# Kernel tuning notes

Measured on AMD Instinct MI355X. Metric: run time of the kernel, lower is better.

Reference implementation:

```python
import jax, jax.numpy as jnp
import numpy as np

TEMPERATURE = 0.1
EPS = 1e-12  # matches torch F.normalize default eps


def setup_inputs() -> dict:
    key = jax.random.key(0)
    k1, k2 = jax.random.split(key)
    B, D = 4096, 512
    features1 = jax.random.normal(k1, (B, D), dtype=jnp.float32)
    features2 = jax.random.normal(k2, (B, D), dtype=jnp.float32)
    return {"features1": features1, "features2": features2}


def _l2_normalize(x, axis=1):
    norm = jnp.linalg.norm(x, axis=axis, keepdims=True)
    return x / jnp.maximum(norm, EPS)


def reference(features1, features2):
    B = features1.shape[0]
    f1 = _l2_normalize(features1)
    f2 = _l2_normalize(features2)
    features = jnp.concatenate([f1, f2], axis=0)  # (2B, D)
    sim = jnp.matmul(features, features.T) / TEMPERATURE  # (2B, 2B)
    # mask self-similarity on the diagonal with -inf
    diag = jnp.eye(2 * B, dtype=bool)
    sim = jnp.where(diag, -jnp.inf, sim)
    # positive pair labels: row i pairs with i+B (first half) / i-B (second half)
    labels = jnp.concatenate([jnp.arange(B) + B, jnp.arange(B)], axis=0)
    log_probs = jax.nn.log_softmax(sim, axis=-1)  # (2B, 2B)
    nll = -jnp.take_along_axis(log_probs, labels[:, None], axis=1)[:, 0]
    return jnp.mean(nll)
```

## Files before the change

kernel.cpp:

```cpp
#include <hip/hip_runtime.h>

#define NROWS 8192
#define HALF_N 4096
#define DIM 512
#define INV_T 10.0f
#define NRB 64
#define NBLOCKS 2080

typedef __attribute__((ext_vector_type(4))) float f32x4;
typedef __attribute__((ext_vector_type(2))) long long2v;

__device__ __forceinline__ void async16(const void* g, void* l) {
  __builtin_amdgcn_global_load_lds(
      (const __attribute__((address_space(1))) unsigned int*)g,
      (__attribute__((address_space(3))) unsigned int*)l, 16, 0, 0);
}

__global__ __launch_bounds__(256) void norm_cast_k(
    const float* __restrict__ f1, const float* __restrict__ f2,
    unsigned char* __restrict__ Fn, float* __restrict__ rowsum) {
  int wave = threadIdx.x >> 6;
  int lane = threadIdx.x & 63;
  int row = blockIdx.x * 4 + wave;
  const float* src = (row < HALF_N) ? (f1 + (size_t)row * DIM)
                                    : (f2 + (size_t)(row - HALF_N) * DIM);
  const float4* p = reinterpret_cast<const float4*>(src + lane * 8);
  float4 v0 = p[0];
  float4 v1 = p[1];
  float ss = v0.x*v0.x + v0.y*v0.y + v0.z*v0.z + v0.w*v0.w
           + v1.x*v1.x + v1.y*v1.y + v1.z*v1.z + v1.w*v1.w;
  #pragma unroll
  for (int off = 1; off < 64; off <<= 1) ss += __shfl_xor(ss, off);
  float scale = 1.0f / fmaxf(sqrtf(ss), 1e-12f);
  int lo = __builtin_amdgcn_cvt_pk_fp8_f32(v0.x * scale, v0.y * scale, 0, false);
  lo = __builtin_amdgcn_cvt_pk_fp8_f32(v0.z * scale, v0.w * scale, lo, true);
  int u = lane & 7;
  int g = lane >> 3;
  int pos = 2 * (u & 3) + (u >> 2);
  *reinterpret_cast<int2*>(Fn + (size_t)row * DIM + g * 64 + pos * 8) =
      make_int2(lo,
                __builtin_amdgcn_cvt_pk_fp8_f32(v1.z * scale, v1.w * scale,
                    __builtin_amdgcn_cvt_pk_fp8_f32(v1.x * scale, v1.y * scale, 0, false),
                    true));
  if (lane == 0) rowsum[row] = 0.0f;
}

__global__ __launch_bounds__(256, 3) void sym_gemm_k(
    const unsigned char* __restrict__ Fn, float* __restrict__ rowsum,
    float* __restrict__ pairsim) {
  int bx = blockIdx.x;
  int gbx = (bx & 7) * (NBLOCKS / 8) + (bx >> 3);
  int rb = 0, rem = gbx;
  while (rem >= NRB - rb) { rem -= NRB - rb; ++rb; }
  const int cb = rb + rem;
  const int row0 = rb * 128, col0 = cb * 128;

  const int tid = threadIdx.x;
  const int wave = tid >> 6;
  const int lane = tid & 63;
  const int quad = lane >> 4;
  const int colid = lane & 15;
  const int wr0 = (wave >> 1) * 64;
  const int wc0 = (wave & 1) * 64;

  __shared__ __align__(16) unsigned char Alds[128 * 64];
  __shared__ __align__(16) unsigned char Blds[128 * 64];
  __shared__ float redrow[128];
  __shared__ float redcol[128];

  if (tid < 128) { redrow[tid] = 0.0f; redcol[tid] = 0.0f; }

  const unsigned char* srcA[2]; const unsigned char* srcB[2];
  unsigned char* dstA[2]; unsigned char* dstB[2];
  #pragma unroll
  for (int seg = 0; seg < 2; ++seg) {
    int inst = wave + seg * 4;
    int r = inst * 16 + (lane >> 2);
    int c = (lane & 3) ^ ((r >> 1) & 3);
    srcA[seg] = Fn + (size_t)(row0 + r) * DIM + c * 16;
    srcB[seg] = Fn + (size_t)(col0 + r) * DIM + c * 16;
    dstA[seg] = Alds + inst * 1024;
    dstB[seg] = Blds + inst * 1024;
  }

  const unsigned char* afp[4]; const unsigned char* bfp[4];
  #pragma unroll
  for (int t = 0; t < 4; ++t) {
    int ra = wr0 + t * 16 + colid;
    int rc = wc0 + t * 16 + colid;
    afp[t] = Alds + ra * 64 + ((quad ^ ((ra >> 1) & 3)) << 4);
    bfp[t] = Blds + rc * 64 + ((quad ^ ((rc >> 1) & 3)) << 4);
  }

  f32x4 acc[4][4];
  #pragma unroll
  for (int t = 0; t < 4; ++t)
    #pragma unroll
    for (int u = 0; u < 4; ++u) acc[t][u] = (f32x4){0.f, 0.f, 0.f, 0.f};

  for (int kc = 0; kc < 8; ++kc) {
    __syncthreads();
    const size_t ko = (size_t)kc * 64;
    #pragma unroll
    for (int seg = 0; seg < 2; ++seg) {
      async16(srcA[seg] + ko, dstA[seg]);
      async16(srcB[seg] + ko, dstB[seg]);
    }
    __syncthreads();

    long2v af[4], bf[4];
    #pragma unroll
    for (int t = 0; t < 4; ++t) af[t] = *reinterpret_cast<const long2v*>(afp[t]);
    #pragma unroll
    for (int u = 0; u < 4; ++u) bf[u] = *reinterpret_cast<const long2v*>(bfp[u]);
    #pragma unroll
    for (int s = 0; s < 2; ++s)
      #pragma unroll
      for (int t = 0; t < 4; ++t)
        #pragma unroll
        for (int u = 0; u < 4; ++u)
          acc[t][u] = __builtin_amdgcn_mfma_f32_16x16x32_fp8_fp8(
              af[t][s], bf[u][s], acc[t][u], 0, 0, 0);
  }

  float re[4][4];
  float ce[4];
  #pragma unroll
  for (int t = 0; t < 4; ++t)
    #pragma unroll
    for (int r = 0; r < 4; ++r) re[t][r] = 0.0f;
  #pragma unroll
  for (int u = 0; u < 4; ++u) ce[u] = 0.0f;

  #pragma unroll
  for (int t = 0; t < 4; ++t) {
    #pragma unroll
    for (int u = 0; u < 4; ++u) {
      f32x4 a = acc[t][u];
      const int gc = col0 + wc0 + u * 16 + colid;
      #pragma unroll
      for (int r = 0; r < 4; ++r) {
        int grow = row0 + wr0 + t * 16 + quad * 4 + r;
        float sim = a[r] * INV_T;
        float e = (gc > grow) ? __expf(sim) : 0.0f;
        re[t][r] += e;
        ce[u] += e;
        if (gc == grow + HALF_N && grow < HALF_N) {
          pairsim[grow] = sim;
          pairsim[gc] = sim;
        }
      }
    }
  }

  #pragma unroll
  for (int t = 0; t < 4; ++t)
    #pragma unroll
    for (int r = 0; r < 4; ++r) {
      float v = re[t][r];
      v += __shfl_xor(v, 1); v += __shfl_xor(v, 2);
      v += __shfl_xor(v, 4); v += __shfl_xor(v, 8);
      if (colid == 0) atomicAdd(&redrow[wr0 + t * 16 + quad * 4 + r], v);
    }
  #pragma unroll
  for (int u = 0; u < 4; ++u) {
    float v = ce[u];
    v += __shfl_xor(v, 16); v += __shfl_xor(v, 32);
    if (lane < 16) atomicAdd(&redcol[wc0 + u * 16 + colid], v);
  }
  __syncthreads();
  if (tid < 128) atomicAdd(&rowsum[row0 + tid], redrow[tid]);
  else           atomicAdd(&rowsum[col0 + tid - 128], redcol[tid - 128]);
}

__global__ __launch_bounds__(1024) void finalize_k(
    const float* __restrict__ rowsum, const float* __restrict__ pairsim,
    float* __restrict__ out) {
  float local = 0.0f;
  for (int i = threadIdx.x; i < NROWS; i += 1024)
    local += logf(rowsum[i]) - pairsim[i];
  #pragma unroll
  for (int off = 1; off < 64; off <<= 1) local += __shfl_xor(local, off);
  __shared__ float red[16];
  int wave = threadIdx.x >> 6;
  int lane = threadIdx.x & 63;
  if (lane == 0) red[wave] = local;
  __syncthreads();
  if (threadIdx.x == 0) {
    float s = 0.0f;
    #pragma unroll
    for (int w = 0; w < 16; ++w) s += red[w];
    out[0] = s * (1.0f / (float)NROWS);
  }
}

extern "C" void kernel_launch(void* const* d_in, const int* in_sizes, int n_in,
                              void* d_out, int out_size, void* d_ws, size_t ws_size,
                              hipStream_t stream) {
  const float* f1 = (const float*)d_in[0];
  const float* f2 = (const float*)d_in[1];
  unsigned char* Fn = (unsigned char*)d_ws;
  float* rowsum = (float*)((char*)d_ws + (size_t)NROWS * DIM);
  float* pairsim = rowsum + NROWS;
  float* out = (float*)d_out;

  norm_cast_k<<<NROWS / 4, 256, 0, stream>>>(f1, f2, Fn, rowsum);
  sym_gemm_k<<<NBLOCKS, 256, 0, stream>>>(Fn, rowsum, pairsim);
  finalize_k<<<1, 1024, 0, stream>>>(rowsum, pairsim, out);
}
```

Before: 104.8 us.

## Double K-chunk per GEMM stage and parallelize finalize reduction with atomics

The symmetric GEMM now loads 128-byte K chunks per stage instead of 64, halving the number of barrier-separated load/compute iterations. It uses a new 8-way XOR swizzle to keep LDS reads conflict-free. The finalize kernel changes from one 1024-thread block to 32 blocks that atomically accumulate into an output zeroed by the normalize kernel. LDS use per block doubles, which may reduce occupancy, and atomic summation makes the final result order-dependent.

```diff
diff --git a/kernel.cpp b/kernel.cpp
--- a/kernel.cpp
+++ b/kernel.cpp
@@ -18,7 +18,8 @@
 
 __global__ __launch_bounds__(256) void norm_cast_k(
     const float* __restrict__ f1, const float* __restrict__ f2,
-    unsigned char* __restrict__ Fn, float* __restrict__ rowsum) {
+    unsigned char* __restrict__ Fn, float* __restrict__ rowsum,
+    float* __restrict__ out) {
   int wave = threadIdx.x >> 6;
   int lane = threadIdx.x & 63;
   int row = blockIdx.x * 4 + wave;
@@ -34,15 +35,15 @@
   float scale = 1.0f / fmaxf(sqrtf(ss), 1e-12f);
   int lo = __builtin_amdgcn_cvt_pk_fp8_f32(v0.x * scale, v0.y * scale, 0, false);
   lo = __builtin_amdgcn_cvt_pk_fp8_f32(v0.z * scale, v0.w * scale, lo, true);
+  int hi = __builtin_amdgcn_cvt_pk_fp8_f32(v1.x * scale, v1.y * scale, 0, false);
+  hi = __builtin_amdgcn_cvt_pk_fp8_f32(v1.z * scale, v1.w * scale, hi, true);
   int u = lane & 7;
   int g = lane >> 3;
   int pos = 2 * (u & 3) + (u >> 2);
   *reinterpret_cast<int2*>(Fn + (size_t)row * DIM + g * 64 + pos * 8) =
-      make_int2(lo,
-                __builtin_amdgcn_cvt_pk_fp8_f32(v1.z * scale, v1.w * scale,
-                    __builtin_amdgcn_cvt_pk_fp8_f32(v1.x * scale, v1.y * scale, 0, false),
-                    true));
+      make_int2(lo, hi);
   if (lane == 0) rowsum[row] = 0.0f;
+  if (blockIdx.x == 0 && threadIdx.x == 0) out[0] = 0.0f;
 }
 
 __global__ __launch_bounds__(256, 3) void sym_gemm_k(
@@ -63,20 +64,20 @@
   const int wr0 = (wave >> 1) * 64;
   const int wc0 = (wave & 1) * 64;
 
-  __shared__ __align__(16) unsigned char Alds[128 * 64];
-  __shared__ __align__(16) unsigned char Blds[128 * 64];
+  __shared__ __align__(128) unsigned char Alds[128 * 128];
+  __shared__ __align__(128) unsigned char Blds[128 * 128];
   __shared__ float redrow[128];
   __shared__ float redcol[128];
 
   if (tid < 128) { redrow[tid] = 0.0f; redcol[tid] = 0.0f; }
 
-  const unsigned char* srcA[2]; const unsigned char* srcB[2];
-  unsigned char* dstA[2]; unsigned char* dstB[2];
-  #pragma unroll
-  for (int seg = 0; seg < 2; ++seg) {
+  const unsigned char* srcA[4]; const unsigned char* srcB[4];
+  unsigned char* dstA[4]; unsigned char* dstB[4];
+  #pragma unroll
+  for (int seg = 0; seg < 4; ++seg) {
     int inst = wave + seg * 4;
-    int r = inst * 16 + (lane >> 2);
-    int c = (lane & 3) ^ ((r >> 1) & 3);
+    int r = inst * 8 + (lane >> 3);
+    int c = (lane & 7) ^ (lane >> 3);
     srcA[seg] = Fn + (size_t)(row0 + r) * DIM + c * 16;
     srcB[seg] = Fn + (size_t)(col0 + r) * DIM + c * 16;
     dstA[seg] = Alds + inst * 1024;
@@ -88,8 +89,8 @@
   for (int t = 0; t < 4; ++t) {
     int ra = wr0 + t * 16 + colid;
     int rc = wc0 + t * 16 + colid;
-    afp[t] = Alds + ra * 64 + ((quad ^ ((ra >> 1) & 3)) << 4);
-    bfp[t] = Blds + rc * 64 + ((quad ^ ((rc >> 1) & 3)) << 4);
+    afp[t] = Alds + ra * 128 + ((quad ^ (ra & 7)) << 4);
+    bfp[t] = Blds + rc * 128 + ((quad ^ (rc & 7)) << 4);
   }
 
   f32x4 acc[4][4];
@@ -98,29 +99,36 @@
     #pragma unroll
     for (int u = 0; u < 4; ++u) acc[t][u] = (f32x4){0.f, 0.f, 0.f, 0.f};
 
-  for (int kc = 0; kc < 8; ++kc) {
+  for (int kc = 0; kc < 4; ++kc) {
     __syncthreads();
-    const size_t ko = (size_t)kc * 64;
-    #pragma unroll
-    for (int seg = 0; seg < 2; ++seg) {
+    const size_t ko = (size_t)kc * 128;
+    #pragma unroll
+    for (int seg = 0; seg < 4; ++seg) {
       async16(srcA[seg] + ko, dstA[seg]);
       async16(srcB[seg] + ko, dstB[seg]);
     }
     __syncthreads();
 
-    long2v af[4], bf[4];
-    #pragma unroll
-    for (int t = 0; t < 4; ++t) af[t] = *reinterpret_cast<const long2v*>(afp[t]);
-    #pragma unroll
-    for (int u = 0; u < 4; ++u) bf[u] = *reinterpret_cast<const long2v*>(bfp[u]);
-    #pragma unroll
-    for (int s = 0; s < 2; ++s)
+    #pragma unroll
+    for (int g = 0; g < 2; ++g) {
+      long2v af[4], bf[4];
       #pragma unroll
       for (int t = 0; t < 4; ++t)
+        af[t] = *reinterpret_cast<const long2v*>(
+            (const unsigned char*)((uintptr_t)afp[t] ^ (g ? 64u : 0u)));
+      #pragma unroll
+      for (int u = 0; u < 4; ++u)
+        bf[u] = *reinterpret_cast<const long2v*>(
+            (const unsigned char*)((uintptr_t)bfp[u] ^ (g ? 64u : 0u)));
+      #pragma unroll
+      for (int s = 0; s < 2; ++s)
         #pragma unroll
-        for (int u = 0; u < 4; ++u)
-          acc[t][u] = __builtin_amdgcn_mfma_f32_16x16x32_fp8_fp8(
-              af[t][s], bf[u][s], acc[t][u], 0, 0, 0);
+        for (int t = 0; t < 4; ++t)
+          #pragma unroll
+          for (int u = 0; u < 4; ++u)
+            acc[t][u] = __builtin_amdgcn_mfma_f32_16x16x32_fp8_fp8(
+                af[t][s], bf[u][s], acc[t][u], 0, 0, 0);
+    }
   }
 
   float re[4][4];
@@ -173,25 +181,15 @@
   else           atomicAdd(&rowsum[col0 + tid - 128], redcol[tid - 128]);
 }
 
-__global__ __launch_bounds__(1024) void finalize_k(
+__global__ __launch_bounds__(256) void finalize_k(
     const float* __restrict__ rowsum, const float* __restrict__ pairsim,
     float* __restrict__ out) {
-  float local = 0.0f;
-  for (int i = threadIdx.x; i < NROWS; i += 1024)
-    local += logf(rowsum[i]) - pairsim[i];
+  int i = blockIdx.x * 256 + threadIdx.x;
+  float local = logf(rowsum[i]) - pairsim[i];
   #pragma unroll
   for (int off = 1; off < 64; off <<= 1) local += __shfl_xor(local, off);
-  __shared__ float red[16];
-  int wave = threadIdx.x >> 6;
-  int lane = threadIdx.x & 63;
-  if (lane == 0) red[wave] = local;
-  __syncthreads();
-  if (threadIdx.x == 0) {
-    float s = 0.0f;
-    #pragma unroll
-    for (int w = 0; w < 16; ++w) s += red[w];
-    out[0] = s * (1.0f / (float)NROWS);
-  }
+  if ((threadIdx.x & 63) == 0)
+    atomicAdd(out, local * (1.0f / (float)NROWS));
 }
 
 extern "C" void kernel_launch(void* const* d_in, const int* in_sizes, int n_in,
@@ -204,7 +202,7 @@
   float* pairsim = rowsum + NROWS;
   float* out = (float*)d_out;
 
-  norm_cast_k<<<NROWS / 4, 256, 0, stream>>>(f1, f2, Fn, rowsum);
+  norm_cast_k<<<NROWS / 4, 256, 0, stream>>>(f1, f2, Fn, rowsum, out);
   sym_gemm_k<<<NBLOCKS, 256, 0, stream>>>(Fn, rowsum, pairsim);
-  finalize_k<<<1, 1024, 0, stream>>>(rowsum, pairsim, out);
-}
+  finalize_k<<<NROWS / 256, 256, 0, stream>>>(rowsum, pairsim, out);
+}
```

Measured after the change: 108.1 us. +3.2%, slower.
